# Performance work log

Measured on AMD Instinct MI355X. Metric: run time of the kernel, lower is better.

## Reference

```python
import jax, jax.numpy as jnp
import numpy as np

V, TB, L, H, D, HD, FF = 50257, 1024, 6, 12, 768, 64, 4 * 768
B, T = 2, 1024
EOS = 50256


def _layernorm(x, g, b, eps=1e-5):
    mu = x.mean(-1, keepdims=True)
    var = ((x - mu) ** 2).mean(-1, keepdims=True)
    return (x - mu) * jax.lax.rsqrt(var + eps) * g + b


def setup_inputs() -> dict:
    key = jax.random.key(0)
    ks = jax.random.split(key, 10)
    resid_std = 0.02 * (2 * L) ** (-0.5)

    def n(k, shape, std=0.02):
        return (std * jax.random.normal(k, shape)).astype(jnp.float32)

    return {
        "idx": jax.random.randint(ks[0], (B, T), 0, V, dtype=jnp.int32),
        "targets": jax.random.randint(ks[1], (B, T), 0, V, dtype=jnp.int32),
        "token_emb": n(ks[2], (V, D)),           # tied with head
        "pos_emb": n(ks[3], (1, TB, D)),
        "ln1_g": jnp.ones((L, D), jnp.float32),
        "ln1_b": jnp.zeros((L, D), jnp.float32),
        "ln2_g": jnp.ones((L, D), jnp.float32),
        "ln2_b": jnp.zeros((L, D), jnp.float32),
        "W_qkv": n(ks[4], (L, D, 3 * D)),
        "b_qkv": jnp.zeros((L, 3 * D), jnp.float32),
        "W_proj": n(ks[5], (L, D, D), resid_std),
        "b_proj": jnp.zeros((L, D), jnp.float32),
        "W_fc1": n(ks[6], (L, D, FF)),
        "b_fc1": jnp.zeros((L, FF), jnp.float32),
        "W_fc2": n(ks[7], (L, FF, D), resid_std),
        "b_fc2": jnp.zeros((L, D), jnp.float32),
        "lnf_g": jnp.ones((D,), jnp.float32),
        "lnf_b": jnp.zeros((D,), jnp.float32),
    }


def reference(idx, targets, token_emb, pos_emb, ln1_g, ln1_b, ln2_g, ln2_b,
              W_qkv, b_qkv, W_proj, b_proj, W_fc1, b_fc1, W_fc2, b_fc2,
              lnf_g, lnf_b):
    Bc, Tc = idx.shape
    x = token_emb[idx] + pos_emb[:, :Tc, :]  # [B,T,D]; dropout=0 -> identity

    # document-boundary causal mask: same_doc & causal
    is_eos = (idx == EOS).astype(jnp.int32)
    doc_id = jnp.cumsum(is_eos, axis=1) - is_eos          # [B,T]
    same_doc = doc_id[:, :, None] == doc_id[:, None, :]   # [B,T,T]
    causal = jnp.tril(jnp.ones((Tc, Tc), dtype=bool))
    mask = same_doc & causal                               # [B,T,T]
    scale = 1.0 / float(np.sqrt(HD))

    def block(x, p):
        g1, b1, Wq, bq, Wp, bp, g2, b2, Wf1, bf1, Wf2, bf2 = p
        h = _layernorm(x, g1, b1)
        qkv = (h @ Wq + bq).reshape(Bc, Tc, 3, H, HD)
        q = qkv[:, :, 0].transpose(0, 2, 1, 3)  # [B,H,T,hd]
        k = qkv[:, :, 1].transpose(0, 2, 1, 3)
        v = qkv[:, :, 2].transpose(0, 2, 1, 3)
        att = jnp.einsum('bhqd,bhkd->bhqk', q, k) * scale
        att = jnp.where(mask[:, None, :, :], att, -jnp.inf)
        att = jax.nn.softmax(att, axis=-1)
        y = jnp.einsum('bhqk,bhkd->bhqd', att, v)
        y = y.transpose(0, 2, 1, 3).reshape(Bc, Tc, D)
        x = x + (y @ Wp + bp)
        h2 = _layernorm(x, g2, b2)
        x = x + (jax.nn.gelu(h2 @ Wf1 + bf1, approximate=False) @ Wf2 + bf2)
        return x, None

    x, _ = jax.lax.scan(block, x, (ln1_g, ln1_b, W_qkv, b_qkv, W_proj, b_proj,
                                   ln2_g, ln2_b, W_fc1, b_fc1, W_fc2, b_fc2))
    x = _layernorm(x, lnf_g, lnf_b)
    logits = x @ token_emb.T  # tied head, no bias
    logp = jax.nn.log_softmax(logits, axis=-1)
    tgt = targets.astype(jnp.int32)[..., None]
    loss = -jnp.take_along_axis(logp, tgt, axis=-1).mean()
    return logits, loss
```

## Files before the change

kernel.cpp:

```cpp
#include <hip/hip_runtime.h>
#include <hip/hip_bf16.h>
#include <math.h>

#define V_ 50257
#define L_ 6
#define H_ 12
#define D_ 768
#define HD_ 64
#define FF_ 3072
#define B_ 2
#define T_ 1024
#define NTOK (B_*T_)
#define EOS_ 50256
#define QBLK 64
#define KVB 64
#define NS2 393
#define QS3 (3*D_)

typedef __attribute__((ext_vector_type(8))) short s16x8;
typedef __attribute__((ext_vector_type(4))) float f32x4;

__device__ __forceinline__ short f2bf(float f) {
  __hip_bfloat16 h = __float2bfloat16(f);
  return *reinterpret_cast<short*>(&h);
}

__device__ __forceinline__ void gl_lds16(const void* g, void* l) {
  __builtin_amdgcn_global_load_lds(
      (const __attribute__((address_space(1))) unsigned int*)g,
      (__attribute__((address_space(3))) unsigned int*)l, 16, 0, 0);
}

__global__ void k_embed(const int* __restrict__ idx, const float* __restrict__ tok,
                        const float* __restrict__ pos, float* __restrict__ x) {
  int gid = blockIdx.x * blockDim.x + threadIdx.x;
  const int total = NTOK * D_;
  if (gid >= total) return;
  int row = gid / D_;
  int d = gid - row * D_;
  int t = row & (T_ - 1);
  x[gid] = tok[(size_t)idx[row] * D_ + d] + pos[t * D_ + d];
}

__global__ void k_docid(const int* __restrict__ idx, int* __restrict__ doc) {
  int b = threadIdx.x;
  if (b >= B_) return;
  int c = 0;
  for (int t = 0; t < T_; ++t) {
    int e = (idx[b*T_ + t] == EOS_) ? 1 : 0;
    doc[b*T_ + t] = c;
    c += e;
  }
}

__global__ void k_cast_tok(const float* __restrict__ in,
                           __hip_bfloat16* __restrict__ out, long n8) {
  long i = (long)blockIdx.x*blockDim.x + threadIdx.x;
  long stride = (long)gridDim.x*blockDim.x;
  for (; i < n8; i += stride) {
    const float4* src = (const float4*)(in + i*8);
    float4 v0 = src[0], v1 = src[1];
    s16x8 s;
    s[0]=f2bf(v0.x); s[1]=f2bf(v0.y); s[2]=f2bf(v0.z); s[3]=f2bf(v0.w);
    s[4]=f2bf(v1.x); s[5]=f2bf(v1.y); s[6]=f2bf(v1.z); s[7]=f2bf(v1.w);
    *(s16x8*)((short*)out + i*8) = s;
  }
}

__global__ void k_ln(const float* __restrict__ x, const float* __restrict__ g,
                     const float* __restrict__ b, __hip_bfloat16* __restrict__ out) {
  int row = blockIdx.x;
  const float* xr = x + (size_t)row * D_;
  int lane = threadIdx.x;
  float vals[D_/64];
  float s = 0.f;
  #pragma unroll
  for (int i = 0; i < D_/64; ++i) { vals[i] = xr[lane + i*64]; s += vals[i]; }
  #pragma unroll
  for (int o = 1; o < 64; o <<= 1) s += __shfl_xor(s, o);
  float mu = s * (1.f/D_);
  float v = 0.f;
  #pragma unroll
  for (int i = 0; i < D_/64; ++i) { float d0 = vals[i]-mu; v += d0*d0; }
  #pragma unroll
  for (int o = 1; o < 64; o <<= 1) v += __shfl_xor(v, o);
  float inv = rsqrtf(v * (1.f/D_) + 1e-5f);
  #pragma unroll
  for (int i = 0; i < D_/64; ++i) {
    int d = lane + i*64;
    out[(size_t)row*D_ + d] = __float2bfloat16((vals[i]-mu)*inv*g[d] + b[d]);
  }
}

__global__ void k_wt(const float* __restrict__ in, __hip_bfloat16* __restrict__ out,
                     int K, int N) {
  __shared__ float tile[32][33];
  int l = blockIdx.z;
  const float* src = in + (size_t)l*K*N;
  __hip_bfloat16* dst = out + (size_t)l*N*K;
  int n0 = blockIdx.x*32, k0 = blockIdx.y*32;
  int tx = threadIdx.x, ty = threadIdx.y;
  #pragma unroll
  for (int i = 0; i < 4; ++i)
    tile[ty + i*8][tx] = src[(size_t)(k0 + ty + i*8)*N + n0 + tx];
  __syncthreads();
  #pragma unroll
  for (int i = 0; i < 4; ++i)
    dst[(size_t)(n0 + ty + i*8)*K + k0 + tx] = __float2bfloat16(tile[tx][ty + i*8]);
}

__global__ __launch_bounds__(512) void k_mfma_nt(
    const __hip_bfloat16* __restrict__ A,
    const __hip_bfloat16* __restrict__ Bh,
    const float* __restrict__ Bf,
    const float* __restrict__ bias,
    const float* resid,
    float* outf, __hip_bfloat16* outh,
    int M, int N, int K, int gelu)
{
  __shared__ __align__(16) short lds_a[2][128*64];
  __shared__ __align__(16) short lds_b[2][128*64];
  const int t = threadIdx.x;
  const int m0 = blockIdx.y * 128;
  const int n0 = blockIdx.x * 128;
  const int lane = t & 63;
  const int wid = t >> 6;
  const int wm = (wid >> 2) * 64;
  const int wn = (wid & 3) * 32;
  const int lrow = lane & 15;
  const int lkb = (lane >> 4) * 16;
  const int wbase = (t & 448) * 16;

  auto stageA = [&](int buf, int k0) {
    #pragma unroll
    for (int p = 0; p < 2; ++p) {
      int c = p*512 + t;
      int row = c >> 3;
      int colb = (c & 7) << 4;
      const char* src = (const char*)A + ((size_t)(m0+row)*K + k0)*2 + (colb ^ ((row & 7) << 4));
      gl_lds16(src, (char*)lds_a[buf] + p*8192 + wbase);
    }
  };
  auto stageB = [&](int buf, int k0) {
    if (Bh) {
      #pragma unroll
      for (int p = 0; p < 2; ++p) {
        int c = p*512 + t;
        int row = c >> 3;
        int colb = (c & 7) << 4;
        const char* src = (const char*)Bh + ((size_t)(n0+row)*K + k0)*2 + (colb ^ ((row & 7) << 4));
        gl_lds16(src, (char*)lds_b[buf] + p*8192 + wbase);
      }
    } else {
      #pragma unroll
      for (int p = 0; p < 2; ++p) {
        int c = p*512 + t;
        int row = c >> 3;
        int colb = (c & 7) << 4;
        int gn = n0 + row;
        s16x8 s = {0,0,0,0,0,0,0,0};
        if (gn < N) {
          const char* src = (const char*)Bf + ((size_t)gn*K + k0)*4 + colb*2;
          float4 v0 = *(const float4*)src;
          float4 v1 = *(const float4*)(src + 16);
          s[0]=f2bf(v0.x); s[1]=f2bf(v0.y); s[2]=f2bf(v0.z); s[3]=f2bf(v0.w);
          s[4]=f2bf(v1.x); s[5]=f2bf(v1.y); s[6]=f2bf(v1.z); s[7]=f2bf(v1.w);
        }
        int dst = (row*128 + colb) ^ ((row & 7) << 4);
        *(s16x8*)((char*)lds_b[buf] + dst) = s;
      }
    }
  };

  f32x4 acc[4][2];
  #pragma unroll
  for (int i = 0; i < 4; ++i)
    #pragma unroll
    for (int j = 0; j < 2; ++j)
      acc[i][j] = (f32x4){0.f, 0.f, 0.f, 0.f};

  const int nk = K >> 6;
  stageA(0, 0); stageB(0, 0);
  stageA(1, 64); stageB(1, 64);
  const bool piped = (Bh != nullptr);
  for (int kt = 0; kt < nk; ++kt) {
    if (piped && kt + 1 < nk) asm volatile("s_waitcnt vmcnt(4)" ::: "memory");
    else                      asm volatile("s_waitcnt vmcnt(0) lgkmcnt(0)" ::: "memory");
    __builtin_amdgcn_s_barrier();
    const int cur = kt & 1;
    #pragma unroll
    for (int ks = 0; ks < 2; ++ks) {
      s16x8 af[4], bfr[2];
      #pragma unroll
      for (int f = 0; f < 4; ++f) {
        int row = wm + f*16 + lrow;
        int off = (row*128 + ks*64 + lkb) ^ ((row & 7) << 4);
        af[f] = *(const s16x8*)((const char*)lds_a[cur] + off);
      }
      #pragma unroll
      for (int f = 0; f < 2; ++f) {
        int row = wn + f*16 + lrow;
        int off = (row*128 + ks*64 + lkb) ^ ((row & 7) << 4);
        bfr[f] = *(const s16x8*)((const char*)lds_b[cur] + off);
      }
      #pragma unroll
      for (int fm = 0; fm < 4; ++fm)
        #pragma unroll
        for (int fn = 0; fn < 2; ++fn)
          acc[fm][fn] = __builtin_amdgcn_mfma_f32_16x16x32_bf16(
              af[fm], bfr[fn], acc[fm][fn], 0, 0, 0);
    }
    __builtin_amdgcn_s_barrier();
    if (kt + 2 < nk) { stageA(cur, (kt+2)*64); stageB(cur, (kt+2)*64); }
  }
  const int crow = (lane >> 4) * 4;
  #pragma unroll
  for (int fm = 0; fm < 4; ++fm) {
    #pragma unroll
    for (int fn = 0; fn < 2; ++fn) {
      int col = n0 + wn + fn*16 + lrow;
      if (col >= N) continue;
      #pragma unroll
      for (int r = 0; r < 4; ++r) {
        int row = m0 + wm + fm*16 + crow + r;
        float v = acc[fm][fn][r];
        if (bias) v += bias[col];
        if (gelu) v = 0.5f * v * (1.f + erff(v * 0.70710678118654752f));
        if (resid) v += resid[(size_t)row*N + col];
        if (outf) outf[(size_t)row*N + col] = v;
        else      outh[(size_t)row*N + col] = __float2bfloat16(v);
      }
    }
  }
}

__global__ __launch_bounds__(256) void k_mfma_nt64(
    const __hip_bfloat16* __restrict__ A,
    const __hip_bfloat16* __restrict__ Bh,
    const float* __restrict__ bias,
    const float* resid,
    float* outf,
    int M, int N, int K)
{
  __shared__ __align__(16) short lds_a[2][64*64];
  __shared__ __align__(16) short lds_b[2][64*64];
  const int t = threadIdx.x;
  const int m0 = blockIdx.y * 64;
  const int n0 = blockIdx.x * 64;
  const int lane = t & 63;
  const int wid = t >> 6;
  const int wm = (wid >> 1) * 32;
  const int wn = (wid & 1) * 32;
  const int lrow = lane & 15;
  const int lkb = (lane >> 4) * 16;
  const int wbase = (t & 192) * 16;

  auto stage = [&](int buf, int k0) {
    #pragma unroll
    for (int p = 0; p < 2; ++p) {
      int c = p*256 + t;
      int row = c >> 3;
      int colb = (c & 7) << 4;
      const char* srcA = (const char*)A + ((size_t)(m0+row)*K + k0)*2 + (colb ^ ((row & 7) << 4));
      gl_lds16(srcA, (char*)lds_a[buf] + p*4096 + wbase);
    }
    #pragma unroll
    for (int p = 0; p < 2; ++p) {
      int c = p*256 + t;
      int row = c >> 3;
      int colb = (c & 7) << 4;
      const char* srcB = (const char*)Bh + ((size_t)(n0+row)*K + k0)*2 + (colb ^ ((row & 7) << 4));
      gl_lds16(srcB, (char*)lds_b[buf] + p*4096 + wbase);
    }
  };

  f32x4 acc[2][2];
  #pragma unroll
  for (int i = 0; i < 2; ++i)
    #pragma unroll
    for (int j = 0; j < 2; ++j)
      acc[i][j] = (f32x4){0.f, 0.f, 0.f, 0.f};

  const int nk = K >> 6;
  stage(0, 0);
  stage(1, 64);
  for (int kt = 0; kt < nk; ++kt) {
    if (kt + 1 < nk) asm volatile("s_waitcnt vmcnt(4)" ::: "memory");
    else             asm volatile("s_waitcnt vmcnt(0)" ::: "memory");
    __builtin_amdgcn_s_barrier();
    const int cur = kt & 1;
    #pragma unroll
    for (int ks = 0; ks < 2; ++ks) {
      s16x8 af[2], bfr[2];
      #pragma unroll
      for (int f = 0; f < 2; ++f) {
        int row = wm + f*16 + lrow;
        int off = (row*128 + ks*64 + lkb) ^ ((row & 7) << 4);
        af[f] = *(const s16x8*)((const char*)lds_a[cur] + off);
      }
      #pragma unroll
      for (int f = 0; f < 2; ++f) {
        int row = wn + f*16 + lrow;
        int off = (row*128 + ks*64 + lkb) ^ ((row & 7) << 4);
        bfr[f] = *(const s16x8*)((const char*)lds_b[cur] + off);
      }
      #pragma unroll
      for (int fm = 0; fm < 2; ++fm)
        #pragma unroll
        for (int fn = 0; fn < 2; ++fn)
          acc[fm][fn] = __builtin_amdgcn_mfma_f32_16x16x32_bf16(
              af[fm], bfr[fn], acc[fm][fn], 0, 0, 0);
    }
    __builtin_amdgcn_s_barrier();
    if (kt + 2 < nk) stage(cur, (kt+2)*64);
  }
  const int crow = (lane >> 4) * 4;
  #pragma unroll
  for (int fm = 0; fm < 2; ++fm) {
    #pragma unroll
    for (int fn = 0; fn < 2; ++fn) {
      int col = n0 + wn + fn*16 + lrow;
      #pragma unroll
      for (int r = 0; r < 4; ++r) {
        int row = m0 + wm + fm*16 + crow + r;
        float v = acc[fm][fn][r] + bias[col];
        if (resid) v += resid[(size_t)row*N + col];
        outf[(size_t)row*N + col] = v;
      }
    }
  }
}

__global__ __launch_bounds__(512) void k_logits(
    const __hip_bfloat16* __restrict__ A,
    const __hip_bfloat16* __restrict__ Bh,
    const float* __restrict__ Bf,
    float* __restrict__ C,
    float2* __restrict__ part)
{
  __shared__ __align__(16) short lds_a[2][128*64];
  __shared__ __align__(16) short lds_b[2][128*64];
  const int t = threadIdx.x;
  const int bid = blockIdx.x;
  const int lid = (bid & 7) * (NS2*16/8) + (bid >> 3);
  const int m0 = (lid & 15) * 128;
  const int nt = lid >> 4;
  const int n0 = nt * 128;
  const int lane = t & 63;
  const int wid = t >> 6;
  const int wm = (wid >> 2) * 64;
  const int wn = (wid & 3) * 32;
  const int lrow = lane & 15;
  const int lkb = (lane >> 4) * 16;
  const int wbase = (t & 448) * 16;

  auto stageA = [&](int buf, int k0) {
    #pragma unroll
    for (int p = 0; p < 2; ++p) {
      int c = p*512 + t;
      int row = c >> 3;
      int colb = (c & 7) << 4;
      const char* src = (const char*)A + ((size_t)(m0+row)*768 + k0)*2 + (colb ^ ((row & 7) << 4));
      gl_lds16(src, (char*)lds_a[buf] + p*8192 + wbase);
    }
  };
  auto stageB = [&](int buf, int k0) {
    if (Bh) {
      #pragma unroll
      for (int p = 0; p < 2; ++p) {
        int c = p*512 + t;
        int row = c >> 3;
        int colb = (c & 7) << 4;
        const char* src = (const char*)Bh + ((size_t)(n0+row)*768 + k0)*2 + (colb ^ ((row & 7) << 4));
        gl_lds16(src, (char*)lds_b[buf] + p*8192 + wbase);
      }
    } else {
      #pragma unroll
      for (int p = 0; p < 2; ++p) {
        int c = p*512 + t;
        int row = c >> 3;
        int colb = (c & 7) << 4;
        int gn = n0 + row;
        s16x8 s = {0,0,0,0,0,0,0,0};
        if (gn < V_) {
          const char* src = (const char*)Bf + ((size_t)gn*768 + k0)*4 + colb*2;
          float4 v0 = *(const float4*)src;
          float4 v1 = *(const float4*)(src + 16);
          s[0]=f2bf(v0.x); s[1]=f2bf(v0.y); s[2]=f2bf(v0.z); s[3]=f2bf(v0.w);
          s[4]=f2bf(v1.x); s[5]=f2bf(v1.y); s[6]=f2bf(v1.z); s[7]=f2bf(v1.w);
        }
        int dst = (row*128 + colb) ^ ((row & 7) << 4);
        *(s16x8*)((char*)lds_b[buf] + dst) = s;
      }
    }
  };

  f32x4 acc[4][2];
  #pragma unroll
  for (int i = 0; i < 4; ++i)
    #pragma unroll
    for (int j = 0; j < 2; ++j)
      acc[i][j] = (f32x4){0.f, 0.f, 0.f, 0.f};

  stageA(0, 0); stageB(0, 0);
  stageA(1, 64); stageB(1, 64);
  const bool piped = (Bh != nullptr);
  for (int kt = 0; kt < 12; ++kt) {
    if (piped && kt + 1 < 12) asm volatile("s_waitcnt vmcnt(4)" ::: "memory");
    else                      asm volatile("s_waitcnt vmcnt(0) lgkmcnt(0)" ::: "memory");
    __builtin_amdgcn_s_barrier();
    const int cur = kt & 1;
    #pragma unroll
    for (int ks = 0; ks < 2; ++ks) {
      s16x8 af[4], bfr[2];
      #pragma unroll
      for (int f = 0; f < 4; ++f) {
        int row = wm + f*16 + lrow;
        int off = (row*128 + ks*64 + lkb) ^ ((row & 7) << 4);
        af[f] = *(const s16x8*)((const char*)lds_a[cur] + off);
      }
      #pragma unroll
      for (int f = 0; f < 2; ++f) {
        int row = wn + f*16 + lrow;
        int off = (row*128 + ks*64 + lkb) ^ ((row & 7) << 4);
        bfr[f] = *(const s16x8*)((const char*)lds_b[cur] + off);
      }
      #pragma unroll
      for (int fm = 0; fm < 4; ++fm)
        #pragma unroll
        for (int fn = 0; fn < 2; ++fn)
          acc[fm][fn] = __builtin_amdgcn_mfma_f32_16x16x32_bf16(
              af[fm], bfr[fn], acc[fm][fn], 0, 0, 0);
    }
    __builtin_amdgcn_s_barrier();
    if (kt + 2 < 12) { stageA(cur, (kt+2)*64); stageB(cur, (kt+2)*64); }
  }
  const int crow = (lane >> 4) * 4;
  bool valid[2];
  #pragma unroll
  for (int fn = 0; fn < 2; ++fn) valid[fn] = (n0 + wn + fn*16 + lrow) < V_;
  float2* red = (float2*)lds_a;
  #pragma unroll
  for (int fm = 0; fm < 4; ++fm) {
    #pragma unroll
    for (int r = 0; r < 4; ++r) {
      int rit = wm + fm*16 + crow + r;
      int row = m0 + rit;
      float m = -1e30f;
      #pragma unroll
      for (int fn = 0; fn < 2; ++fn) {
        if (valid[fn]) {
          float v = acc[fm][fn][r];
          C[(size_t)row*V_ + n0 + wn + fn*16 + lrow] = v;
          m = fmaxf(m, v);
        }
      }
      #pragma unroll
      for (int o = 1; o < 16; o <<= 1) m = fmaxf(m, __shfl_xor(m, o));
      float s = 0.f;
      #pragma unroll
      for (int fn = 0; fn < 2; ++fn)
        if (valid[fn]) s += __expf(acc[fm][fn][r] - m);
      #pragma unroll
      for (int o = 1; o < 16; o <<= 1) s += __shfl_xor(s, o);
      if (lrow == 0) red[rit*4 + (wid & 3)] = make_float2(m, s);
    }
  }
  __syncthreads();
  if (t < 128) {
    float M = -1e30f, S = 0.f;
    #pragma unroll
    for (int wc = 0; wc < 4; ++wc) {
      float2 p = red[t*4 + wc];
      float mn = fmaxf(M, p.x);
      S = S*__expf(M - mn) + p.y*__expf(p.x - mn);
      M = mn;
    }
    part[(size_t)(m0 + t)*NS2 + nt] = make_float2(M, S);
  }
}

__global__ void k_rowloss2(const float2* __restrict__ part,
                           const float* __restrict__ logits,
                           const int* __restrict__ tgt, float* __restrict__ rl) {
  int row = blockIdx.x;
  int lane = threadIdx.x;
  float M = -1e30f, S = 0.f;
  for (int i = lane; i < NS2; i += 64) {
    float2 p = part[(size_t)row*NS2 + i];
    float mn = fmaxf(M, p.x);
    S = S*__expf(M - mn) + p.y*__expf(p.x - mn);
    M = mn;
  }
  #pragma unroll
  for (int o = 1; o < 64; o <<= 1) {
    float Mo = __shfl_xor(M, o);
    float So = __shfl_xor(S, o);
    float mn = fmaxf(M, Mo);
    S = S*__expf(M - mn) + So*__expf(Mo - mn);
    M = mn;
  }
  if (lane == 0)
    rl[row] = (logf(S) + M) - logits[(size_t)row*V_ + tgt[row]];
}

__global__ __launch_bounds__(256) void k_fattn(
    const __hip_bfloat16* __restrict__ qkv, const int* __restrict__ doc,
    __hip_bfloat16* __restrict__ y)
{
  __shared__ __align__(16) short q_lds[QBLK*64];
  __shared__ __align__(16) short k_lds[KVB*64];
  __shared__ __align__(16) short vt_lds[64*KVB];
  __shared__ __align__(16) short p_lds[4][16*64];
  __shared__ int doc_k[KVB];
  const int t = threadIdx.x;
  const int lane = t & 63;
  const int w = t >> 6;
  const int q0 = (gridDim.x - 1 - blockIdx.x) * QBLK;
  const int h = blockIdx.y, b = blockIdx.z;
  const int lrow = lane & 15;
  const int lgrp = lane >> 4;
  const int crow = lgrp * 4;
  const int wbase = (t & 192) * 16;
  const short* qp = (const short*)qkv;

  #pragma unroll
  for (int p = 0; p < 2; ++p) {
    int c = p*256 + t;
    int row = c >> 3;
    int colb = (c & 7) << 4;
    const char* src = (const char*)(qp + ((size_t)(b*T_ + q0 + row))*QS3 + h*HD_)
                      + (colb ^ ((row & 7) << 4));
    gl_lds16(src, (char*)q_lds + p*4096 + wbase);
  }
  int docq[4];
  #pragma unroll
  for (int r = 0; r < 4; ++r)
    docq[r] = doc[b*T_ + q0 + w*16 + crow + r];
  __syncthreads();

  float m_r[4], l_r[4];
  #pragma unroll
  for (int r = 0; r < 4; ++r) { m_r[r] = -1e30f; l_r[r] = 0.f; }
  f32x4 o[4];
  #pragma unroll
  for (int fd = 0; fd < 4; ++fd) o[fd] = (f32x4){0.f,0.f,0.f,0.f};

  const int ntiles = q0/KVB + 1;
  for (int kt = 0; kt < ntiles; ++kt) {
    const int kv0 = kt * KVB;
    #pragma unroll
    for (int p = 0; p < 2; ++p) {
      int c = p*256 + t;
      int row = c >> 3;
      int colb = (c & 7) << 4;
      const char* src = (const char*)(qp + ((size_t)(b*T_ + kv0 + row))*QS3 + D_ + h*HD_)
                        + (colb ^ ((row & 7) << 4));
      gl_lds16(src, (char*)k_lds + p*4096 + wbase);
    }
    #pragma unroll
    for (int p = 0; p < 2; ++p) {
      int c = p*256 + t;
      int kvr = c >> 3, d0 = (c & 7)*8;
      s16x8 s = *(const s16x8*)(qp + ((size_t)(b*T_ + kv0 + kvr))*QS3 + 2*D_ + h*HD_ + d0);
      #pragma unroll
      for (int j = 0; j < 8; ++j) {
        int d = d0 + j;
        int off = (d*128 + kvr*2) ^ ((d & 7) << 4);
        *(short*)((char*)vt_lds + off) = s[j];
      }
    }
    if (t < KVB) doc_k[t] = doc[b*T_ + kv0 + t];
    __syncthreads();

    f32x4 sfr[4];
    #pragma unroll
    for (int fn = 0; fn < 4; ++fn) sfr[fn] = (f32x4){0.f,0.f,0.f,0.f};
    #pragma unroll
    for (int ks = 0; ks < 2; ++ks) {
      int arow = w*16 + lrow;
      s16x8 af = *(const s16x8*)((const char*)q_lds +
                 ((arow*128 + lgrp*16 + ks*64) ^ ((arow & 7) << 4)));
      #pragma unroll
      for (int fn = 0; fn < 4; ++fn) {
        int brow = fn*16 + lrow;
        s16x8 bf = *(const s16x8*)((const char*)k_lds +
                   ((brow*128 + lgrp*16 + ks*64) ^ ((brow & 7) << 4)));
        sfr[fn] = __builtin_amdgcn_mfma_f32_16x16x32_bf16(af, bf, sfr[fn], 0, 0, 0);
      }
    }
    int dk[4];
    #pragma unroll
    for (int fn = 0; fn < 4; ++fn) dk[fn] = doc_k[fn*16 + lrow];
    float rowmax[4] = {-1e30f, -1e30f, -1e30f, -1e30f};
    #pragma unroll
    for (int fn = 0; fn < 4; ++fn) {
      int col = kv0 + fn*16 + lrow;
      #pragma unroll
      for (int r = 0; r < 4; ++r) {
        int qrow = q0 + w*16 + crow + r;
        bool ok = (col <= qrow) && (dk[fn] == docq[r]);
        float v = ok ? sfr[fn][r] * 0.125f : -1e30f;
        sfr[fn][r] = v;
        rowmax[r] = fmaxf(rowmax[r], v);
      }
    }
    #pragma unroll
    for (int r = 0; r < 4; ++r) {
      float v = rowmax[r];
      #pragma unroll
      for (int off = 1; off < 16; off <<= 1) v = fmaxf(v, __shfl_xor(v, off));
      rowmax[r] = v;
    }
    float alpha[4], psum[4];
    #pragma unroll
    for (int r = 0; r < 4; ++r) {
      float mn = fmaxf(m_r[r], rowmax[r]);
      alpha[r] = __expf(m_r[r] - mn);
      m_r[r] = mn;
      psum[r] = 0.f;
    }
    #pragma unroll
    for (int fn = 0; fn < 4; ++fn) {
      #pragma unroll
      for (int r = 0; r < 4; ++r) {
        float sv = sfr[fn][r];
        float p = (sv < -5e29f) ? 0.f : __expf(sv - m_r[r]);
        psum[r] += p;
        int rl_ = crow + r;
        int off = (rl_*128 + (fn*16 + lrow)*2) ^ ((rl_ & 7) << 4);
        *(short*)((char*)p_lds[w] + off) = f2bf(p);
      }
    }
    #pragma unroll
    for (int r = 0; r < 4; ++r) {
      float v = psum[r];
      #pragma unroll
      for (int off = 1; off < 16; off <<= 1) v += __shfl_xor(v, off);
      l_r[r] = l_r[r]*alpha[r] + v;
    }
    #pragma unroll
    for (int fd = 0; fd < 4; ++fd)
      #pragma unroll
      for (int r = 0; r < 4; ++r)
        o[fd][r] *= alpha[r];
    #pragma unroll
    for (int ks = 0; ks < 2; ++ks) {
      s16x8 af = *(const s16x8*)((const char*)p_lds[w] +
                 ((lrow*128 + lgrp*16 + ks*64) ^ ((lrow & 7) << 4)));
      #pragma unroll
      for (int fd = 0; fd < 4; ++fd) {
        int brow = fd*16 + lrow;
        s16x8 bf = *(const s16x8*)((const char*)vt_lds +
                   ((brow*128 + lgrp*16 + ks*64) ^ ((brow & 7) << 4)));
        o[fd] = __builtin_amdgcn_mfma_f32_16x16x32_bf16(af, bf, o[fd], 0, 0, 0);
      }
    }
    __syncthreads();
  }
  #pragma unroll
  for (int r = 0; r < 4; ++r) {
    float inv = 1.f / l_r[r];
    int rowg = b*T_ + q0 + w*16 + crow + r;
    #pragma unroll
    for (int fd = 0; fd < 4; ++fd) {
      int col = h*HD_ + fd*16 + lrow;
      y[(size_t)rowg*D_ + col] = __float2bfloat16(o[fd][r] * inv);
    }
  }
}

__global__ void k_rowloss(const float* __restrict__ logits,
                          const int* __restrict__ tgt, float* __restrict__ rl) {
  __shared__ float red[4];
  int row = blockIdx.x;
  const float* lr = logits + (size_t)row * V_;
  int tid = threadIdx.x;
  float m = -1e30f;
  for (int v = tid; v < V_; v += 256) m = fmaxf(m, lr[v]);
  #pragma unroll
  for (int o = 1; o < 64; o <<= 1) m = fmaxf(m, __shfl_xor(m, o));
  if ((tid & 63) == 0) red[tid >> 6] = m;
  __syncthreads();
  m = fmaxf(fmaxf(red[0], red[1]), fmaxf(red[2], red[3]));
  __syncthreads();
  float s = 0.f;
  for (int v = tid; v < V_; v += 256) s += __expf(lr[v] - m);
  #pragma unroll
  for (int o = 1; o < 64; o <<= 1) s += __shfl_xor(s, o);
  if ((tid & 63) == 0) red[tid >> 6] = s;
  __syncthreads();
  if (tid == 0) {
    s = red[0]+red[1]+red[2]+red[3];
    rl[row] = (logf(s) + m) - lr[tgt[row]];
  }
}

__global__ void k_loss(const float* __restrict__ rl, float* __restrict__ out) {
  __shared__ float red[4];
  int tid = threadIdx.x;
  float s = 0.f;
  for (int i = tid; i < NTOK; i += 256) s += rl[i];
  #pragma unroll
  for (int o = 1; o < 64; o <<= 1) s += __shfl_xor(s, o);
  if ((tid & 63) == 0) red[tid >> 6] = s;
  __syncthreads();
  if (tid == 0) {
    s = red[0]+red[1]+red[2]+red[3];
    out[0] = s / (float)NTOK;
  }
}

extern "C" void kernel_launch(void* const* d_in, const int* in_sizes, int n_in,
                              void* d_out, int out_size, void* d_ws, size_t ws_size,
                              hipStream_t stream) {
  const int*   idx   = (const int*)d_in[0];
  const int*   tgt   = (const int*)d_in[1];
  const float* tok   = (const float*)d_in[2];
  const float* pos   = (const float*)d_in[3];
  const float* ln1_g = (const float*)d_in[4];
  const float* ln1_b = (const float*)d_in[5];
  const float* ln2_g = (const float*)d_in[6];
  const float* ln2_b = (const float*)d_in[7];
  const float* W_qkv = (const float*)d_in[8];
  const float* b_qkv = (const float*)d_in[9];
  const float* W_proj= (const float*)d_in[10];
  const float* b_proj= (const float*)d_in[11];
  const float* W_fc1 = (const float*)d_in[12];
  const float* b_fc1 = (const float*)d_in[13];
  const float* W_fc2 = (const float*)d_in[14];
  const float* b_fc2 = (const float*)d_in[15];
  const float* lnf_g = (const float*)d_in[16];
  const float* lnf_b = (const float*)d_in[17];

  float* out = (float*)d_out;

  char* ob = (char*)d_out;
  float*           x    = (float*)(ob + 0);
  __hip_bfloat16*  qkv  = (__hip_bfloat16*)(ob + (size_t)6291456);
  __hip_bfloat16*  y    = (__hip_bfloat16*)(ob + (size_t)15728640);
  __hip_bfloat16*  tff  = (__hip_bfloat16*)(ob + (size_t)18874368);
  __hip_bfloat16*  WTq  = (__hip_bfloat16*)(ob + (size_t)40894464);
  __hip_bfloat16*  WTp  = (__hip_bfloat16*)(ob + (size_t)62128128);
  __hip_bfloat16*  WT1  = (__hip_bfloat16*)(ob + (size_t)69206016);
  __hip_bfloat16*  WT2  = (__hip_bfloat16*)(ob + (size_t)97517568);

  char* wb = (char*)d_ws;
  __hip_bfloat16* h    = (__hip_bfloat16*)(wb + 0);
  int*    doc  = (int*)  (wb + (size_t)3145728);
  float*  rl   = (float*)(wb + (size_t)3153920);
  float2* part = (float2*)(wb + (size_t)3162112);
  __hip_bfloat16* tokh = (__hip_bfloat16*)(wb + (size_t)9601024);
  const size_t ws_need_part = (size_t)9601024;
  const size_t ws_need_tokh = (size_t)9601024 + 77194752 + 131072;
  const bool fused_loss = (ws_size >= ws_need_part);
  const bool use_tokh   = (ws_size >= ws_need_tokh);

  dim3 tb(32, 8);
  k_wt<<<dim3(2304/32, 768/32, L_), tb, 0, stream>>>(W_qkv,  WTq,  768, 2304);
  k_wt<<<dim3( 768/32, 768/32, L_), tb, 0, stream>>>(W_proj, WTp,  768,  768);
  k_wt<<<dim3(3072/32, 768/32, L_), tb, 0, stream>>>(W_fc1,  WT1,  768, 3072);
  k_wt<<<dim3( 768/32,3072/32, L_), tb, 0, stream>>>(W_fc2,  WT2, 3072,  768);
  if (use_tokh)
    k_cast_tok<<<2048, 256, 0, stream>>>(tok, tokh, (long)V_*768/8);

  k_embed<<<(NTOK*D_ + 255)/256, 256, 0, stream>>>(idx, tok, pos, x);
  k_docid<<<1, 64, 0, stream>>>(idx, doc);

  for (int l = 0; l < L_; ++l) {
    k_ln<<<NTOK, 64, 0, stream>>>(x, ln1_g + l*D_, ln1_b + l*D_, h);
    k_mfma_nt<<<dim3(2304/128, NTOK/128), 512, 0, stream>>>(
        h, WTq + (size_t)l*2304*768, nullptr, b_qkv + (size_t)l*2304, nullptr,
        nullptr, qkv, NTOK, 2304, 768, 0);
    k_fattn<<<dim3(T_/QBLK, H_, B_), 256, 0, stream>>>(qkv, doc, y);
    k_mfma_nt64<<<dim3(768/64, NTOK/64), 256, 0, stream>>>(
        y, WTp + (size_t)l*768*768, b_proj + (size_t)l*768, x, x,
        NTOK, 768, 768);
    k_ln<<<NTOK, 64, 0, stream>>>(x, ln2_g + l*D_, ln2_b + l*D_, h);
    k_mfma_nt<<<dim3(3072/128, NTOK/128), 512, 0, stream>>>(
        h, WT1 + (size_t)l*3072*768, nullptr, b_fc1 + (size_t)l*3072, nullptr,
        nullptr, tff, NTOK, 3072, 768, 1);
    k_mfma_nt64<<<dim3(768/64, NTOK/64), 256, 0, stream>>>(
        tff, WT2 + (size_t)l*768*3072, b_fc2 + (size_t)l*768, x, x,
        NTOK, 768, 3072);
  }
  k_ln<<<NTOK, 64, 0, stream>>>(x, lnf_g, lnf_b, h);

  if (fused_loss) {
    k_logits<<<NS2*16, 512, 0, stream>>>(
        h, use_tokh ? tokh : nullptr, tok, out, part);
    k_rowloss2<<<NTOK, 64, 0, stream>>>(part, out, tgt, rl);
  } else {
    k_mfma_nt<<<dim3((V_ + 127)/128, NTOK/128), 512, 0, stream>>>(
        h, nullptr, tok, nullptr, nullptr, out, nullptr, NTOK, V_, 768, 0);
    k_rowloss<<<NTOK, 256, 0, stream>>>(out, tgt, rl);
  }
  k_loss<<<1, 256, 0, stream>>>(rl, out + (size_t)NTOK*V_);
}
```

Baseline: 1.499 ms.

## Double-buffer K/V tiles in flash attention with register-prefetched V

The flash-attention kernel now double-buffers K and V^T in shared memory. It issues the async K load and the register loads of V for the next tile before computing the current one, and uses explicit vmcnt waits with raw barriers in place of __syncthreads. The whole per-batch doc-id array is loaded into LDS once instead of per tile. This is meant to hide global memory latency behind MFMA work, at the cost of more LDS and registers, which may lower occupancy. It also relies on hand-counted vmcnt values being correct.

```diff
diff --git a/kernel.cpp b/kernel.cpp
--- a/kernel.cpp
+++ b/kernel.cpp
@@ -509,10 +509,10 @@
     __hip_bfloat16* __restrict__ y)
 {
   __shared__ __align__(16) short q_lds[QBLK*64];
-  __shared__ __align__(16) short k_lds[KVB*64];
-  __shared__ __align__(16) short vt_lds[64*KVB];
+  __shared__ __align__(16) short k_lds[2][KVB*64];
+  __shared__ __align__(16) short vt_lds[2][64*KVB];
   __shared__ __align__(16) short p_lds[4][16*64];
-  __shared__ int doc_k[KVB];
+  __shared__ int doc_lds[T_];
   const int t = threadIdx.x;
   const int lane = t & 63;
   const int w = t >> 6;
@@ -524,6 +524,18 @@
   const int wbase = (t & 192) * 16;
   const short* qp = (const short*)qkv;
 
+  auto stageK = [&](int kv0, int buf) {
+    #pragma unroll
+    for (int p = 0; p < 2; ++p) {
+      int c = p*256 + t;
+      int row = c >> 3;
+      int colb = (c & 7) << 4;
+      const char* src = (const char*)(qp + ((size_t)(b*T_ + kv0 + row))*QS3 + D_ + h*HD_)
+                        + (colb ^ ((row & 7) << 4));
+      gl_lds16(src, (char*)k_lds[buf] + p*4096 + wbase);
+    }
+  };
+
   #pragma unroll
   for (int p = 0; p < 2; ++p) {
     int c = p*256 + t;
@@ -533,11 +545,21 @@
                       + (colb ^ ((row & 7) << 4));
     gl_lds16(src, (char*)q_lds + p*4096 + wbase);
   }
+  #pragma unroll
+  for (int i = 0; i < 4; ++i) doc_lds[t + i*256] = doc[b*T_ + t + i*256];
+  stageK(0, 0);
+  s16x8 vc0, vc1;
+  {
+    int c0 = t, c1 = 256 + t;
+    vc0 = *(const s16x8*)(qp + ((size_t)(b*T_ + (c0>>3)))*QS3 + 2*D_ + h*HD_ + (c0&7)*8);
+    vc1 = *(const s16x8*)(qp + ((size_t)(b*T_ + (c1>>3)))*QS3 + 2*D_ + h*HD_ + (c1&7)*8);
+  }
+  __syncthreads();
+
   int docq[4];
   #pragma unroll
   for (int r = 0; r < 4; ++r)
-    docq[r] = doc[b*T_ + q0 + w*16 + crow + r];
-  __syncthreads();
+    docq[r] = doc_lds[q0 + w*16 + crow + r];
 
   float m_r[4], l_r[4];
   #pragma unroll
@@ -549,29 +571,34 @@
   const int ntiles = q0/KVB + 1;
   for (int kt = 0; kt < ntiles; ++kt) {
     const int kv0 = kt * KVB;
-    #pragma unroll
-    for (int p = 0; p < 2; ++p) {
-      int c = p*256 + t;
-      int row = c >> 3;
-      int colb = (c & 7) << 4;
-      const char* src = (const char*)(qp + ((size_t)(b*T_ + kv0 + row))*QS3 + D_ + h*HD_)
-                        + (colb ^ ((row & 7) << 4));
-      gl_lds16(src, (char*)k_lds + p*4096 + wbase);
-    }
-    #pragma unroll
-    for (int p = 0; p < 2; ++p) {
-      int c = p*256 + t;
-      int kvr = c >> 3, d0 = (c & 7)*8;
-      s16x8 s = *(const s16x8*)(qp + ((size_t)(b*T_ + kv0 + kvr))*QS3 + 2*D_ + h*HD_ + d0);
+    const int cur = kt & 1;
+    const bool hn = (kt + 1 < ntiles);
+    s16x8 vn0, vn1;
+    if (hn) {
+      stageK(kv0 + KVB, cur ^ 1);
+      int c0 = t, c1 = 256 + t;
+      vn0 = *(const s16x8*)(qp + ((size_t)(b*T_ + kv0 + KVB + (c0>>3)))*QS3 + 2*D_ + h*HD_ + (c0&7)*8);
+      vn1 = *(const s16x8*)(qp + ((size_t)(b*T_ + kv0 + KVB + (c1>>3)))*QS3 + 2*D_ + h*HD_ + (c1&7)*8);
+    }
+    {
+      int c0 = t, kvr0 = c0 >> 3, d00 = (c0 & 7)*8;
       #pragma unroll
       for (int j = 0; j < 8; ++j) {
-        int d = d0 + j;
-        int off = (d*128 + kvr*2) ^ ((d & 7) << 4);
-        *(short*)((char*)vt_lds + off) = s[j];
-      }
-    }
-    if (t < KVB) doc_k[t] = doc[b*T_ + kv0 + t];
-    __syncthreads();
+        int d = d00 + j;
+        int off = (d*128 + kvr0*2) ^ ((d & 7) << 4);
+        *(short*)((char*)vt_lds[cur] + off) = vc0[j];
+      }
+      int c1 = 256 + t, kvr1 = c1 >> 3, d01 = (c1 & 7)*8;
+      #pragma unroll
+      for (int j = 0; j < 8; ++j) {
+        int d = d01 + j;
+        int off = (d*128 + kvr1*2) ^ ((d & 7) << 4);
+        *(short*)((char*)vt_lds[cur] + off) = vc1[j];
+      }
+    }
+    if (hn) asm volatile("s_waitcnt vmcnt(4)" ::: "memory");
+    else    asm volatile("s_waitcnt vmcnt(0)" ::: "memory");
+    __builtin_amdgcn_s_barrier();
 
     f32x4 sfr[4];
     #pragma unroll
@@ -584,14 +611,14 @@
       #pragma unroll
       for (int fn = 0; fn < 4; ++fn) {
         int brow = fn*16 + lrow;
-        s16x8 bf = *(const s16x8*)((const char*)k_lds +
+        s16x8 bf = *(const s16x8*)((const char*)k_lds[cur] +
                    ((brow*128 + lgrp*16 + ks*64) ^ ((brow & 7) << 4)));
         sfr[fn] = __builtin_amdgcn_mfma_f32_16x16x32_bf16(af, bf, sfr[fn], 0, 0, 0);
       }
     }
     int dk[4];
     #pragma unroll
-    for (int fn = 0; fn < 4; ++fn) dk[fn] = doc_k[fn*16 + lrow];
+    for (int fn = 0; fn < 4; ++fn) dk[fn] = doc_lds[kv0 + fn*16 + lrow];
     float rowmax[4] = {-1e30f, -1e30f, -1e30f, -1e30f};
     #pragma unroll
     for (int fn = 0; fn < 4; ++fn) {
@@ -651,12 +678,13 @@
       #pragma unroll
       for (int fd = 0; fd < 4; ++fd) {
         int brow = fd*16 + lrow;
-        s16x8 bf = *(const s16x8*)((const char*)vt_lds +
+        s16x8 bf = *(const s16x8*)((const char*)vt_lds[cur] +
                    ((brow*128 + lgrp*16 + ks*64) ^ ((brow & 7) << 4)));
         o[fd] = __builtin_amdgcn_mfma_f32_16x16x32_bf16(af, bf, o[fd], 0, 0, 0);
       }
     }
-    __syncthreads();
+    __builtin_amdgcn_s_barrier();
+    vc0 = vn0; vc1 = vn1;
   }
   #pragma unroll
   for (int r = 0; r < 4; ++r) {
```

Measured after the change: 1.500 ms. About the same (+0.0%).
